# Kernel optimization log

Measured on AMD Instinct MI355X. Metric: run time of the kernel, lower is better.

The kernel has to match this reference:

```python
import jax, jax.numpy as jnp
import numpy as np

N = 50000      # nodes
E = 800000     # edges
F_IN = 128     # input node feature dim
H = 4          # attention heads
DH = 64        # per-head hidden dim
HID = H * DH   # 256
NEG_SLOPE = 0.2


def gat_conv(h, src, dst, W, al, ar, b, res):
    # DGL GATConv: project, compute attention logits, edge softmax over dst, aggregate.
    feat = (h @ W).reshape(N, H, DH)                      # [N,H,DH]
    el = jnp.einsum('nhd,hd->nh', feat, al)               # [N,H]
    er = jnp.einsum('nhd,hd->nh', feat, ar)               # [N,H]
    e = el[src] + er[dst]                                 # [E,H]
    e = jnp.where(e > 0, e, NEG_SLOPE * e)                # LeakyReLU(0.2)
    m = jax.ops.segment_max(e, dst, num_segments=N)       # [N,H]
    m = jnp.where(jnp.isfinite(m), m, 0.0)                # zero-in-degree safety
    ex = jnp.exp(e - m[dst])                              # [E,H]
    denom = jax.ops.segment_sum(ex, dst, num_segments=N)  # [N,H]
    alpha = ex / jnp.maximum(denom[dst], 1e-16)           # edge softmax
    out = jax.ops.segment_sum(feat[src] * alpha[:, :, None], dst, num_segments=N)
    return out + res.reshape(N, H, DH) + b.reshape(1, H, DH)


def setup_inputs() -> dict:
    key = jax.random.key(0)
    ks = jax.random.split(key, 16)
    x = jax.random.normal(ks[0], (N, F_IN), jnp.float32)
    edge_index = jax.random.randint(ks[1], (2, E), 0, N)
    s_in = 1.0 / np.sqrt(F_IN)
    s_h = 1.0 / np.sqrt(HID)
    W0 = jax.random.normal(ks[2], (F_IN, HID), jnp.float32) * s_in
    W1 = jax.random.normal(ks[3], (HID, HID), jnp.float32) * s_h
    W2 = jax.random.normal(ks[4], (HID, HID), jnp.float32) * s_h
    al0 = jax.random.normal(ks[5], (H, DH), jnp.float32) * 0.1
    al1 = jax.random.normal(ks[6], (H, DH), jnp.float32) * 0.1
    al2 = jax.random.normal(ks[7], (H, DH), jnp.float32) * 0.1
    ar0 = jax.random.normal(ks[8], (H, DH), jnp.float32) * 0.1
    ar1 = jax.random.normal(ks[9], (H, DH), jnp.float32) * 0.1
    ar2 = jax.random.normal(ks[10], (H, DH), jnp.float32) * 0.1
    b0 = jnp.zeros((HID,), jnp.float32)
    b1 = jnp.zeros((HID,), jnp.float32)
    b2 = jnp.zeros((HID,), jnp.float32)
    resW0 = jax.random.normal(ks[11], (F_IN, HID), jnp.float32) * s_in
    return {"x": x, "edge_index": edge_index,
            "W0": W0, "W1": W1, "W2": W2,
            "al0": al0, "al1": al1, "al2": al2,
            "ar0": ar0, "ar1": ar1, "ar2": ar2,
            "b0": b0, "b1": b1, "b2": b2,
            "resW0": resW0}


def reference(x, edge_index, W0, W1, W2, al0, al1, al2, ar0, ar1, ar2, b0, b1, b2, resW0):
    src, dst = edge_index[0], edge_index[1]
    # layer 0: residual via linear projection (in != heads*hidden)
    h = gat_conv(x, src, dst, W0, al0, ar0, b0, x @ resW0).reshape(N, HID)
    h = jax.nn.relu(h)
    # layer 1: identity residual
    h = gat_conv(h, src, dst, W1, al1, ar1, b1, h).reshape(N, HID)
    h = jax.nn.relu(h)
    # layer 2: identity residual, mean over heads
    h = gat_conv(h, src, dst, W2, al2, ar2, b2, h)
    return h.mean(axis=1)  # [N, DH]
```

## Files before the change

kernel.cpp:

```cpp
#include <hip/hip_runtime.h>
#include <math.h>

#define N_NODES 50000
#define N_EDGES 800000
#define F_INPUT 128
#define HEADS 4
#define DHID 64
#define HID 256
#define M_PAD 50048
#define SCAN_B 49

typedef _Float16 half8 __attribute__((ext_vector_type(8)));
typedef _Float16 half4 __attribute__((ext_vector_type(4)));
typedef float f32x4 __attribute__((ext_vector_type(4)));


#define EB_BLOCKS ((N_EDGES + 255) / 256)
#define PREP_A 1600000
#define PREP_B (PREP_A + 196608)
#define PREP_C (PREP_B + 10240)
#define PB_BLOCKS ((PREP_C + 255) / 256)

__global__ void hist_prep_kernel(const int* __restrict__ dst, int* __restrict__ counts,
                                 const float* __restrict__ x, _Float16* __restrict__ x16,
                                 const float* __restrict__ W0, const float* __restrict__ WR,
                                 _Float16* __restrict__ WtL0,
                                 const float* __restrict__ W1, _Float16* __restrict__ Wt1,
                                 const float* __restrict__ W2, _Float16* __restrict__ Wt2,
                                 const float* __restrict__ al0, const float* __restrict__ ar0,
                                 const float* __restrict__ al1, const float* __restrict__ ar1,
                                 const float* __restrict__ al2, const float* __restrict__ ar2) {
    if (blockIdx.x < EB_BLOCKS) {
        int e = blockIdx.x * 256 + threadIdx.x;
        if (e < N_EDGES) atomicAdd(&counts[dst[e]], 1);
        return;
    }
    int t = (blockIdx.x - EB_BLOCKS) * 256 + threadIdx.x;
    if (t < PREP_A) {
        f32x4 v = *(const f32x4*)&x[t * 4];
        half4 h = {(_Float16)v.x, (_Float16)v.y, (_Float16)v.z, (_Float16)v.w};
        *(half4*)&x16[(size_t)t * 4] = h;
    } else if (t < PREP_B) {
        int u = t - PREP_A;
        if (u < 65536) {
            int c = u >> 7;
            int k = u & 127;
            float v = (c < 256) ? W0[k * 256 + c] : WR[k * 256 + (c - 256)];
            WtL0[u] = (_Float16)v;
        } else if (u < 131072) {
            int w = u - 65536;
            int c = w >> 8;
            int k = w & 255;
            Wt1[w] = (_Float16)W1[k * 256 + c];
        } else {
            int w = u - 131072;
            int c = w >> 8;
            int k = w & 255;
            Wt2[w] = (_Float16)W2[k * 256 + c];
        }
    } else if (t < PREP_C) {
        int u = t - PREP_B;
        if (u < 2048) {
            int row8 = u >> 7, k = u & 127;
            int h = row8 & 3;
            const float* vec = (row8 < 4) ? al0 : ar0;
            float s = 0.f;
            for (int d = 0; d < 64; d++) s += W0[k * 256 + h * 64 + d] * vec[h * 64 + d];
            WtL0[(512 + row8) * 128 + k] = (_Float16)s;
        } else if (u < 6144) {
            int w = u - 2048;
            int row8 = w >> 8, k = w & 255;
            int h = row8 & 3;
            const float* vec = (row8 < 4) ? al1 : ar1;
            float s = 0.f;
            for (int d = 0; d < 64; d++) s += W1[k * 256 + h * 64 + d] * vec[h * 64 + d];
            Wt1[(256 + row8) * 256 + k] = (_Float16)s;
        } else {
            int w = u - 6144;
            int row8 = w >> 8, k = w & 255;
            int h = row8 & 3;
            const float* vec = (row8 < 4) ? al2 : ar2;
            float s = 0.f;
            for (int d = 0; d < 64; d++) s += W2[k * 256 + h * 64 + d] * vec[h * 64 + d];
            Wt2[(256 + row8) * 256 + k] = (_Float16)s;
        }
    }
}


__global__ __launch_bounds__(256) void scan1_kernel(const int* __restrict__ counts,
                                                    int* __restrict__ pre,
                                                    int* __restrict__ bsum) {
    __shared__ int buf[256];
    int tid = threadIdx.x;
    int idx = blockIdx.x * 1024 + tid * 4;
    int v0 = 0, v1 = 0, v2 = 0, v3 = 0;
    if (idx + 3 < N_NODES) {
        int4 v = *(const int4*)&counts[idx];
        v0 = v.x; v1 = v.y; v2 = v.z; v3 = v.w;
    } else {
        if (idx + 0 < N_NODES) v0 = counts[idx + 0];
        if (idx + 1 < N_NODES) v1 = counts[idx + 1];
        if (idx + 2 < N_NODES) v2 = counts[idx + 2];
    }
    int s0 = v0, s1 = s0 + v1, s2 = s1 + v2, s3 = s2 + v3;
    buf[tid] = s3;
    __syncthreads();
    for (int off = 1; off < 256; off <<= 1) {
        int t = (tid >= off) ? buf[tid - off] : 0;
        __syncthreads();
        buf[tid] += t;
        __syncthreads();
    }
    int excl = buf[tid] - s3;
    if (idx + 0 < N_NODES) pre[idx + 0] = excl + s0;
    if (idx + 1 < N_NODES) pre[idx + 1] = excl + s1;
    if (idx + 2 < N_NODES) pre[idx + 2] = excl + s2;
    if (idx + 3 < N_NODES) pre[idx + 3] = excl + s3;
    if (tid == 255) bsum[blockIdx.x] = buf[255];
}

__global__ __launch_bounds__(256) void scan23_kernel(const int* __restrict__ pre,
                                                     const int* __restrict__ bsum,
                                                     int* __restrict__ row_ptr) {
    __shared__ int bq[64];
    int tid = threadIdx.x;
    if (tid < 64) {
        int v = (tid < SCAN_B) ? bsum[tid] : 0;
        int orig = v;
#pragma unroll
        for (int off = 1; off < 64; off <<= 1) {
            int t = __shfl_up(v, off, 64);
            if (tid >= off) v += t;
        }
        bq[tid] = v - orig;
    }
    __syncthreads();
    int add = bq[blockIdx.x];
    int idx = blockIdx.x * 1024 + tid * 4;
#pragma unroll
    for (int u = 0; u < 4; u++) {
        int i = idx + u;
        if (i < N_NODES) row_ptr[i + 1] = pre[i] + add;
    }
    if (blockIdx.x == 0 && tid == 0) row_ptr[0] = 0;
}

__global__ void scatter_kernel(const int* __restrict__ src, const int* __restrict__ dst,
                               const int* __restrict__ row_ptr, int* __restrict__ cursor,
                               int* __restrict__ esrc) {
    int e = blockIdx.x * 256 + threadIdx.x;
    if (e < N_EDGES) {
        int d = dst[e];
        int pos = row_ptr[d] + atomicAdd(&cursor[d], 1);
        esrc[pos] = src[e];
    }
}


__device__ __forceinline__ void gl2lds16(const void* g, void* l) {
    __builtin_amdgcn_global_load_lds((const __attribute__((address_space(1))) void*)g,
                                     (__attribute__((address_space(3))) void*)l, 16, 0, 0);
}

__global__ __launch_bounds__(512) void gemm_l0(const _Float16* __restrict__ A16,
                                               const _Float16* __restrict__ WtL0,
                                               _Float16* __restrict__ feat16,
                                               _Float16* __restrict__ res16,
                                               float* __restrict__ el, float* __restrict__ er) {
    __shared__ __align__(16) _Float16 As[4 * 512];
    __shared__ __align__(16) _Float16 Ws[33 * 512];
    int tid = threadIdx.x;
    int w = tid >> 6;
    int lane = tid & 63;
    int lrow = lane & 15;
    int lk = lane >> 4;
    int row0 = blockIdx.x * 64;

    f32x4 acc[4][4] = {};
    f32x4 acc5[4] = {};

    for (int k0 = 0; k0 < F_INPUT; k0 += 32) {
        if (w < 4)
            gl2lds16(A16 + (size_t)(row0 + w * 16 + lrow) * F_INPUT + k0 + lk * 8, &As[w * 512]);
#pragma unroll
        for (int i = 0; i < 4; i++) {
            int tt = i * 8 + w;
            gl2lds16(WtL0 + (size_t)(tt * 16 + lrow) * F_INPUT + k0 + lk * 8, &Ws[tt * 512]);
        }
        if (w == 7)
            gl2lds16(WtL0 + (size_t)(512 + lrow) * F_INPUT + k0 + lk * 8, &Ws[32 * 512]);
        __syncthreads();
        half8 a[4], b[4], b5;
#pragma unroll
        for (int m = 0; m < 4; m++) a[m] = *(const half8*)&As[m * 512 + lane * 8];
#pragma unroll
        for (int j = 0; j < 4; j++) b[j] = *(const half8*)&Ws[(w * 4 + j) * 512 + lane * 8];
        if (w == 3) b5 = *(const half8*)&Ws[32 * 512 + lane * 8];
#pragma unroll
        for (int m = 0; m < 4; m++)
#pragma unroll
            for (int j = 0; j < 4; j++)
                acc[m][j] = __builtin_amdgcn_mfma_f32_16x16x32_f16(a[m], b[j], acc[m][j], 0, 0, 0);
        if (w == 3) {
#pragma unroll
            for (int m = 0; m < 4; m++)
                acc5[m] = __builtin_amdgcn_mfma_f32_16x16x32_f16(a[m], b5, acc5[m], 0, 0, 0);
        }
        __syncthreads();
    }

    if (w < 4) {
#pragma unroll
        for (int m = 0; m < 4; m++) {
#pragma unroll
            for (int r = 0; r < 4; r++) {
                int row = row0 + m * 16 + lk * 4 + r;
                if (row < N_NODES) {
#pragma unroll
                    for (int j = 0; j < 4; j++)
                        feat16[(size_t)row * HID + w * 64 + j * 16 + lrow] = (_Float16)acc[m][j][r];
                }
            }
        }
        if (w == 3 && lrow < 8) {
#pragma unroll
            for (int m = 0; m < 4; m++) {
#pragma unroll
                for (int r = 0; r < 4; r++) {
                    int row = row0 + m * 16 + lk * 4 + r;
                    if (row < N_NODES) {
                        float v = acc5[m][r];
                        if (lrow < 4) el[row * 4 + lrow] = v;
                        else          er[row * 4 + (lrow - 4)] = v;
                    }
                }
            }
        }
    } else {
        int wc = w - 4;
#pragma unroll
        for (int m = 0; m < 4; m++) {
#pragma unroll
            for (int r = 0; r < 4; r++) {
                int row = row0 + m * 16 + lk * 4 + r;
                if (row < N_NODES) {
#pragma unroll
                    for (int j = 0; j < 4; j++)
                        res16[(size_t)row * HID + wc * 64 + j * 16 + lrow] = (_Float16)acc[m][j][r];
                }
            }
        }
    }
}

__global__ __launch_bounds__(512) void gemm_h(const _Float16* __restrict__ A16,
                                              const _Float16* __restrict__ Wt,
                                              _Float16* __restrict__ feat16,
                                              float* __restrict__ el, float* __restrict__ er) {
    __shared__ __align__(16) _Float16 As[8 * 2 * 512];
    __shared__ __align__(16) _Float16 Ws[17 * 2 * 512];
    int tid = threadIdx.x;
    int w = tid >> 6;
    int lane = tid & 63;
    int lrow = lane & 15;
    int lk = lane >> 4;
    int wrow = w >> 2;
    int wcol = w & 3;
    int row0 = blockIdx.x * 128;

    f32x4 acc[4][4] = {};
    f32x4 acc5[4] = {};

    for (int k0 = 0; k0 < HID; k0 += 64) {
#pragma unroll
        for (int c = 0; c < 2; c++) {
            int kk = k0 + c * 32 + lk * 8;
            gl2lds16(A16 + (size_t)(row0 + w * 16 + lrow) * HID + kk, &As[(w * 2 + c) * 512]);
            gl2lds16(Wt + (size_t)(w * 16 + lrow) * HID + kk, &Ws[(w * 2 + c) * 512]);
            gl2lds16(Wt + (size_t)((w + 8) * 16 + lrow) * HID + kk, &Ws[((w + 8) * 2 + c) * 512]);
            if (w == 0)
                gl2lds16(Wt + (size_t)(256 + lrow) * HID + kk, &Ws[(16 * 2 + c) * 512]);
        }
        __syncthreads();
#pragma unroll
        for (int c = 0; c < 2; c++) {
            half8 a[4], b[4], b5;
#pragma unroll
            for (int m = 0; m < 4; m++)
                a[m] = *(const half8*)&As[((wrow * 4 + m) * 2 + c) * 512 + lane * 8];
#pragma unroll
            for (int j = 0; j < 4; j++)
                b[j] = *(const half8*)&Ws[((wcol * 4 + j) * 2 + c) * 512 + lane * 8];
            if (wcol == 3) b5 = *(const half8*)&Ws[(16 * 2 + c) * 512 + lane * 8];
#pragma unroll
            for (int m = 0; m < 4; m++)
#pragma unroll
                for (int j = 0; j < 4; j++)
                    acc[m][j] = __builtin_amdgcn_mfma_f32_16x16x32_f16(a[m], b[j], acc[m][j], 0, 0, 0);
            if (wcol == 3) {
#pragma unroll
                for (int m = 0; m < 4; m++)
                    acc5[m] = __builtin_amdgcn_mfma_f32_16x16x32_f16(a[m], b5, acc5[m], 0, 0, 0);
            }
        }
        __syncthreads();
    }

#pragma unroll
    for (int m = 0; m < 4; m++) {
#pragma unroll
        for (int r = 0; r < 4; r++) {
            int row = row0 + wrow * 64 + m * 16 + lk * 4 + r;
            if (row < N_NODES) {
#pragma unroll
                for (int j = 0; j < 4; j++)
                    feat16[(size_t)row * HID + wcol * 64 + j * 16 + lrow] = (_Float16)acc[m][j][r];
            }
        }
    }
    if (wcol == 3 && lrow < 8) {
#pragma unroll
        for (int m = 0; m < 4; m++) {
#pragma unroll
            for (int r = 0; r < 4; r++) {
                int row = row0 + wrow * 64 + m * 16 + lk * 4 + r;
                if (row < N_NODES) {
                    float v = acc5[m][r];
                    if (lrow < 4) el[row * 4 + lrow] = v;
                    else          er[row * 4 + (lrow - 4)] = v;
                }
            }
        }
    }
}


__global__ __launch_bounds__(256) void agg_kernel(const _Float16* __restrict__ feat16,
                                                  const float* __restrict__ el,
                                                  const float* __restrict__ er,
                                                  const int* __restrict__ row_ptr,
                                                  const int* __restrict__ esrc,
                                                  const _Float16* __restrict__ res16,
                                                  const float* __restrict__ bias,
                                                  _Float16* __restrict__ out16,
                                                  float* __restrict__ outmean,
                                                  int do_relu) {
    __shared__ float lds[4][4 * 65 + 64];
    int wv = threadIdx.x >> 6;
    int lane = threadIdx.x & 63;
    int n = blockIdx.x * 4 + wv;
    int li = lane & 31;
    int sub = lane >> 5;
    int head = li >> 3;
    int start = row_ptr[n];
    int deg = row_ptr[n + 1] - start;
    f32x4 ern = *(const f32x4*)&er[n * 4];
    float* L = lds[wv];
    float* Loff = L + 4 * 65;
    const float* Lex = L + head * 65;

    f32x4 accA = {0.f, 0.f, 0.f, 0.f};
    f32x4 accB = {0.f, 0.f, 0.f, 0.f};
    f32x4 sm4 = {0.f, 0.f, 0.f, 0.f};
    const char* fbase = (const char*)feat16 + li * 16;

    for (int base = 0; base < deg; base += 64) {
        int e = base + lane;
        f32x4 ex4 = {0.f, 0.f, 0.f, 0.f};
        int off = 0;
        if (e < deg) {
            int s = esrc[start + e];
            off = s * (HID * 2);
            f32x4 v = *(const f32x4*)&el[s * 4];
            v = v + ern;
            v.x = v.x > 0.f ? v.x : 0.2f * v.x;
            v.y = v.y > 0.f ? v.y : 0.2f * v.y;
            v.z = v.z > 0.f ? v.z : 0.2f * v.z;
            v.w = v.w > 0.f ? v.w : 0.2f * v.w;
            ex4.x = __expf(v.x);
            ex4.y = __expf(v.y);
            ex4.z = __expf(v.z);
            ex4.w = __expf(v.w);
        }
        L[0 * 65 + lane] = ex4.x;
        L[1 * 65 + lane] = ex4.y;
        L[2 * 65 + lane] = ex4.z;
        L[3 * 65 + lane] = ex4.w;
        Loff[lane] = __int_as_float(off);
        sm4 += ex4;

        int cnt = min(64, deg - base);
        int cnt16 = (cnt + 15) & ~15;
        for (int j = 0; j < cnt16; j += 16) {
            float ex[8]; int o[8];
#pragma unroll
            for (int u = 0; u < 8; u++) {
                int e2 = j + u * 2 + sub;
                ex[u] = Lex[e2];
                o[u] = __float_as_int(Loff[e2]);
            }
            half8 f[8];
#pragma unroll
            for (int u = 0; u < 8; u++) f[u] = *(const half8*)(fbase + o[u]);
#pragma unroll
            for (int u = 0; u < 8; u++) {
                accA.x += ex[u] * (float)f[u][0];
                accA.y += ex[u] * (float)f[u][1];
                accA.z += ex[u] * (float)f[u][2];
                accA.w += ex[u] * (float)f[u][3];
                accB.x += ex[u] * (float)f[u][4];
                accB.y += ex[u] * (float)f[u][5];
                accB.z += ex[u] * (float)f[u][6];
                accB.w += ex[u] * (float)f[u][7];
            }
        }
    }

    accA.x += __shfl_xor(accA.x, 32, 64);
    accA.y += __shfl_xor(accA.y, 32, 64);
    accA.z += __shfl_xor(accA.z, 32, 64);
    accA.w += __shfl_xor(accA.w, 32, 64);
    accB.x += __shfl_xor(accB.x, 32, 64);
    accB.y += __shfl_xor(accB.y, 32, 64);
    accB.z += __shfl_xor(accB.z, 32, 64);
    accB.w += __shfl_xor(accB.w, 32, 64);

#pragma unroll
    for (int off2 = 1; off2 < 64; off2 <<= 1) {
        sm4.x += __shfl_xor(sm4.x, off2, 64);
        sm4.y += __shfl_xor(sm4.y, off2, 64);
        sm4.z += __shfl_xor(sm4.z, off2, 64);
        sm4.w += __shfl_xor(sm4.w, off2, 64);
    }
    float smh = (head == 0) ? sm4.x : (head == 1) ? sm4.y : (head == 2) ? sm4.z : sm4.w;
    float inv = 1.f / fmaxf(smh, 1e-16f);
    accA *= inv;
    accB *= inv;

    half8 rv = *(const half8*)&res16[(size_t)n * HID + li * 8];
    f32x4 bvA = *(const f32x4*)&bias[li * 8];
    f32x4 bvB = *(const f32x4*)&bias[li * 8 + 4];
    accA.x += (float)rv[0] + bvA.x;
    accA.y += (float)rv[1] + bvA.y;
    accA.z += (float)rv[2] + bvA.z;
    accA.w += (float)rv[3] + bvA.w;
    accB.x += (float)rv[4] + bvB.x;
    accB.y += (float)rv[5] + bvB.y;
    accB.z += (float)rv[6] + bvB.z;
    accB.w += (float)rv[7] + bvB.w;
    if (do_relu) {
        accA.x = fmaxf(accA.x, 0.f); accA.y = fmaxf(accA.y, 0.f);
        accA.z = fmaxf(accA.z, 0.f); accA.w = fmaxf(accA.w, 0.f);
        accB.x = fmaxf(accB.x, 0.f); accB.y = fmaxf(accB.y, 0.f);
        accB.z = fmaxf(accB.z, 0.f); accB.w = fmaxf(accB.w, 0.f);
    }
    if (outmean) {
#pragma unroll
        for (int st = 8; st <= 16; st <<= 1) {
            accA.x += __shfl_xor(accA.x, st, 64);
            accA.y += __shfl_xor(accA.y, st, 64);
            accA.z += __shfl_xor(accA.z, st, 64);
            accA.w += __shfl_xor(accA.w, st, 64);
            accB.x += __shfl_xor(accB.x, st, 64);
            accB.y += __shfl_xor(accB.y, st, 64);
            accB.z += __shfl_xor(accB.z, st, 64);
            accB.w += __shfl_xor(accB.w, st, 64);
        }
        if (sub == 0 && li < 8) {
            f32x4 moA = accA * 0.25f;
            f32x4 moB = accB * 0.25f;
            *(f32x4*)&outmean[(size_t)n * DHID + li * 8] = moA;
            *(f32x4*)&outmean[(size_t)n * DHID + li * 8 + 4] = moB;
        }
    } else {
        if (sub == 0) {
            half8 h = {(_Float16)accA.x, (_Float16)accA.y, (_Float16)accA.z, (_Float16)accA.w,
                       (_Float16)accB.x, (_Float16)accB.y, (_Float16)accB.z, (_Float16)accB.w};
            *(half8*)&out16[(size_t)n * HID + li * 8] = h;
        }
    }
}


extern "C" void kernel_launch(void* const* d_in, const int* in_sizes, int n_in,
                              void* d_out, int out_size, void* d_ws, size_t ws_size,
                              hipStream_t stream) {
    const float* x     = (const float*)d_in[0];
    const int*   ei    = (const int*)d_in[1];
    const float* W0    = (const float*)d_in[2];
    const float* W1    = (const float*)d_in[3];
    const float* W2    = (const float*)d_in[4];
    const float* al0   = (const float*)d_in[5];
    const float* al1   = (const float*)d_in[6];
    const float* al2   = (const float*)d_in[7];
    const float* ar0   = (const float*)d_in[8];
    const float* ar1   = (const float*)d_in[9];
    const float* ar2   = (const float*)d_in[10];
    const float* b0    = (const float*)d_in[11];
    const float* b1    = (const float*)d_in[12];
    const float* b2    = (const float*)d_in[13];
    const float* resW0 = (const float*)d_in[14];
    float* out = (float*)d_out;

    const int* srcp = ei;
    const int* dstp = ei + N_EDGES;

    char* p = (char*)d_ws;
    auto alloc = [&](size_t bytes) -> char* {
        char* r = p;
        p += (bytes + 255) & ~(size_t)255;
        return r;
    };
    _Float16*  h16    = (_Float16*)alloc((size_t)M_PAD * HID * 2);
    _Float16*  feat16 = (_Float16*)alloc((size_t)M_PAD * HID * 2);
    _Float16*  res0   = (_Float16*)alloc((size_t)N_NODES * HID * 2);
    _Float16*  x16    = (_Float16*)alloc((size_t)M_PAD * F_INPUT * 2);
    float*     el     = (float*)alloc((size_t)N_NODES * HEADS * 4);
    float*     er     = (float*)alloc((size_t)N_NODES * HEADS * 4);
    _Float16*  WtL0   = (_Float16*)alloc((size_t)528 * F_INPUT * 2);
    _Float16*  Wt1    = (_Float16*)alloc((size_t)272 * HID * 2);
    _Float16*  Wt2    = (_Float16*)alloc((size_t)272 * HID * 2);
    int*       counts = (int*)alloc((size_t)2 * N_NODES * 4);
    int*       cursor = counts + N_NODES;
    int*       rowptr = (int*)alloc((size_t)(N_NODES + 1) * 4);
    int*       esrc   = (int*)alloc((size_t)N_EDGES * 4);
    int*       pre    = (int*)alloc((size_t)N_NODES * 4);
    int*       bsum   = (int*)alloc((size_t)SCAN_B * 4);

    const int NB = N_NODES / 4;

    hipMemsetAsync(counts, 0, (size_t)2 * N_NODES * 4, stream);
    hist_prep_kernel<<<EB_BLOCKS + PB_BLOCKS, 256, 0, stream>>>(
        dstp, counts, x, x16, W0, resW0, WtL0, W1, Wt1, W2, Wt2,
        al0, ar0, al1, ar1, al2, ar2);
    scan1_kernel<<<SCAN_B, 256, 0, stream>>>(counts, pre, bsum);
    scan23_kernel<<<SCAN_B, 256, 0, stream>>>(pre, bsum, rowptr);
    scatter_kernel<<<EB_BLOCKS, 256, 0, stream>>>(srcp, dstp, rowptr, cursor, esrc);

    gemm_l0<<<M_PAD / 64, 512, 0, stream>>>(x16, WtL0, feat16, res0, el, er);
    agg_kernel<<<NB, 256, 0, stream>>>(feat16, el, er, rowptr, esrc, res0, b0, h16, nullptr, 1);

    gemm_h<<<M_PAD / 128, 512, 0, stream>>>(h16, Wt1, feat16, el, er);
    agg_kernel<<<NB, 256, 0, stream>>>(feat16, el, er, rowptr, esrc, h16, b1, h16, nullptr, 1);

    gemm_h<<<M_PAD / 128, 512, 0, stream>>>(h16, Wt2, feat16, el, er);
    agg_kernel<<<NB, 256, 0, stream>>>(feat16, el, er, rowptr, esrc, h16, b2, nullptr, out, 0);
}
```

Baseline: 480.3 us.

## Record edge ranks in histogram and fuse CSR scatter into layer-0 GEMM launch

The histogram pass now stores each edge's atomicAdd return value as its rank within its destination bucket. This lets the scatter write esrc positions directly from row_ptr plus rank, with no second atomic pass over a cursor array. The scatter blocks are merged into the layer-0 GEMM launch as extra leading blocks, removing one kernel launch and letting scatter and GEMM overlap. It adds an 800K-int rank buffer (write then read), and the scatter blocks now run at 512 threads with the GEMM's LDS reservation, which may limit their occupancy.

```diff
diff --git a/kernel.cpp b/kernel.cpp
--- a/kernel.cpp
+++ b/kernel.cpp
@@ -22,6 +22,7 @@
 #define PB_BLOCKS ((PREP_C + 255) / 256)
 
 __global__ void hist_prep_kernel(const int* __restrict__ dst, int* __restrict__ counts,
+                                 int* __restrict__ rank,
                                  const float* __restrict__ x, _Float16* __restrict__ x16,
                                  const float* __restrict__ W0, const float* __restrict__ WR,
                                  _Float16* __restrict__ WtL0,
@@ -32,7 +33,7 @@
                                  const float* __restrict__ al2, const float* __restrict__ ar2) {
     if (blockIdx.x < EB_BLOCKS) {
         int e = blockIdx.x * 256 + threadIdx.x;
-        if (e < N_EDGES) atomicAdd(&counts[dst[e]], 1);
+        if (e < N_EDGES) rank[e] = atomicAdd(&counts[dst[e]], 1);
         return;
     }
     int t = (blockIdx.x - EB_BLOCKS) * 256 + threadIdx.x;
@@ -146,28 +147,31 @@
     if (blockIdx.x == 0 && tid == 0) row_ptr[0] = 0;
 }
 
-__global__ void scatter_kernel(const int* __restrict__ src, const int* __restrict__ dst,
-                               const int* __restrict__ row_ptr, int* __restrict__ cursor,
-                               int* __restrict__ esrc) {
-    int e = blockIdx.x * 256 + threadIdx.x;
-    if (e < N_EDGES) {
-        int d = dst[e];
-        int pos = row_ptr[d] + atomicAdd(&cursor[d], 1);
-        esrc[pos] = src[e];
-    }
-}
-
 
 __device__ __forceinline__ void gl2lds16(const void* g, void* l) {
     __builtin_amdgcn_global_load_lds((const __attribute__((address_space(1))) void*)g,
                                      (__attribute__((address_space(3))) void*)l, 16, 0, 0);
 }
 
-__global__ __launch_bounds__(512) void gemm_l0(const _Float16* __restrict__ A16,
-                                               const _Float16* __restrict__ WtL0,
-                                               _Float16* __restrict__ feat16,
-                                               _Float16* __restrict__ res16,
-                                               float* __restrict__ el, float* __restrict__ er) {
+
+#define SC_B ((N_EDGES + 511) / 512)
+#define GB0 (M_PAD / 64)
+
+__global__ __launch_bounds__(512) void scat_gemm0_kernel(
+        const int* __restrict__ src, const int* __restrict__ dst,
+        const int* __restrict__ row_ptr, const int* __restrict__ rank,
+        int* __restrict__ esrc,
+        const _Float16* __restrict__ A16, const _Float16* __restrict__ WtL0,
+        _Float16* __restrict__ feat16, _Float16* __restrict__ res16,
+        float* __restrict__ el, float* __restrict__ er) {
+    if (blockIdx.x < SC_B) {
+        int e = blockIdx.x * 512 + threadIdx.x;
+        if (e < N_EDGES) {
+            int d = dst[e];
+            esrc[row_ptr[d] + rank[e]] = src[e];
+        }
+        return;
+    }
     __shared__ __align__(16) _Float16 As[4 * 512];
     __shared__ __align__(16) _Float16 Ws[33 * 512];
     int tid = threadIdx.x;
@@ -175,7 +179,7 @@
     int lane = tid & 63;
     int lrow = lane & 15;
     int lk = lane >> 4;
-    int row0 = blockIdx.x * 64;
+    int row0 = (blockIdx.x - SC_B) * 64;
 
     f32x4 acc[4][4] = {};
     f32x4 acc5[4] = {};
@@ -521,8 +525,8 @@
     _Float16*  WtL0   = (_Float16*)alloc((size_t)528 * F_INPUT * 2);
     _Float16*  Wt1    = (_Float16*)alloc((size_t)272 * HID * 2);
     _Float16*  Wt2    = (_Float16*)alloc((size_t)272 * HID * 2);
-    int*       counts = (int*)alloc((size_t)2 * N_NODES * 4);
-    int*       cursor = counts + N_NODES;
+    int*       counts = (int*)alloc((size_t)N_NODES * 4);
+    int*       rank   = (int*)alloc((size_t)N_EDGES * 4);
     int*       rowptr = (int*)alloc((size_t)(N_NODES + 1) * 4);
     int*       esrc   = (int*)alloc((size_t)N_EDGES * 4);
     int*       pre    = (int*)alloc((size_t)N_NODES * 4);
@@ -530,15 +534,15 @@
 
     const int NB = N_NODES / 4;
 
-    hipMemsetAsync(counts, 0, (size_t)2 * N_NODES * 4, stream);
+    hipMemsetAsync(counts, 0, (size_t)N_NODES * 4, stream);
     hist_prep_kernel<<<EB_BLOCKS + PB_BLOCKS, 256, 0, stream>>>(
-        dstp, counts, x, x16, W0, resW0, WtL0, W1, Wt1, W2, Wt2,
+        dstp, counts, rank, x, x16, W0, resW0, WtL0, W1, Wt1, W2, Wt2,
         al0, ar0, al1, ar1, al2, ar2);
     scan1_kernel<<<SCAN_B, 256, 0, stream>>>(counts, pre, bsum);
     scan23_kernel<<<SCAN_B, 256, 0, stream>>>(pre, bsum, rowptr);
-    scatter_kernel<<<EB_BLOCKS, 256, 0, stream>>>(srcp, dstp, rowptr, cursor, esrc);
-
-    gemm_l0<<<M_PAD / 64, 512, 0, stream>>>(x16, WtL0, feat16, res0, el, er);
+
+    scat_gemm0_kernel<<<SC_B + GB0, 512, 0, stream>>>(
+        srcp, dstp, rowptr, rank, esrc, x16, WtL0, feat16, res0, el, er);
     agg_kernel<<<NB, 256, 0, stream>>>(feat16, el, er, rowptr, esrc, res0, b0, h16, nullptr, 1);
 
     gemm_h<<<M_PAD / 128, 512, 0, stream>>>(h16, Wt1, feat16, el, er);
```

Measured after the change: 446.6 us. -7.0%, faster.
